# Kernel tuning notes

Measured on AMD Instinct MI355X. Metric: run time of the kernel, lower is better.

## Reference

```python
import jax, jax.numpy as jnp
import numpy as np

B, S, D, H = 2, 2048, 768, 12
DK = D // H
NEG = -10000.0


def setup_inputs() -> dict:
    key = jax.random.key(0)
    ks = jax.random.split(key, 12)
    def lin(k):
        kw, kb = jax.random.split(k)
        return (jax.random.normal(kw, (D, D), jnp.float32) * 0.02,
                jax.random.normal(kb, (D,), jnp.float32) * 0.02)
    Wq, bq = lin(ks[0]); Wk, bk = lin(ks[1]); Wv, bv = lin(ks[2]); Wo, bo = lin(ks[3])
    query = jax.random.normal(ks[4], (B, S, D), jnp.float32)
    key_t = jax.random.normal(ks[5], (B, S, D), jnp.float32)
    value = jax.random.normal(ks[6], (B, S, D), jnp.float32)
    # causal mask, broadcastable to [B,H,S,S]; positions with 0 are masked
    mask = jnp.tril(jnp.ones((S, S), jnp.int32))[None, None, :, :]
    return {"query": query, "key": key_t, "value": value, "mask": mask,
            "Wq": Wq, "bq": bq, "Wk": Wk, "bk": bk, "Wv": Wv, "bv": bv,
            "Wo": Wo, "bo": bo}


def reference(query, key, value, mask, Wq, bq, Wk, bk, Wv, bv, Wo, bo):
    # torch.nn.Linear: y = x @ W^T + b
    def split_heads(x):  # [B,S,D] -> [B,H,S,DK]
        return x.reshape(B, S, H, DK).transpose(0, 2, 1, 3)
    q = split_heads(query @ Wq.T + bq)
    k = split_heads(key @ Wk.T + bk)
    v = split_heads(value @ Wv.T + bv)
    scores = jnp.einsum('bhqd,bhkd->bhqk', q, k) / jnp.sqrt(jnp.float32(DK))
    scores = jnp.where(mask == 0, NEG, scores)  # masked_fill(mask==0, -1e4)
    attn = jax.nn.softmax(scores, axis=-1)      # dropout p=0.0 -> identity
    x = jnp.einsum('bhqk,bhkd->bhqd', attn, v)  # [B,H,S,DK]
    x = x.transpose(0, 2, 1, 3).reshape(B, S, D)
    return x @ Wo.T + bo
```

## Files before the change

kernel.cpp:

```cpp
#include <hip/hip_runtime.h>
#include <cstdint>


#define B_ 2
#define S_ 2048
#define D_ 768
#define H_ 12
#define DK_ 64

typedef __bf16 bf16;
typedef __bf16 bf16x8 __attribute__((ext_vector_type(8)));
typedef float f32x4 __attribute__((ext_vector_type(4)));
typedef uint32_t u32x4 __attribute__((ext_vector_type(4)));
typedef uint16_t u16x4 __attribute__((ext_vector_type(4)));

__device__ __forceinline__ f32x4 mfma16(bf16x8 a, bf16x8 b, f32x4 c) {
  return __builtin_amdgcn_mfma_f32_16x16x32_bf16(a, b, c, 0, 0, 0);
}

__device__ __forceinline__ void gl2lds16(const bf16* g, bf16* l) {
  __builtin_amdgcn_global_load_lds(
      (const __attribute__((address_space(1))) uint32_t*)g,
      (__attribute__((address_space(3))) uint32_t*)l, 16, 0, 0);
}

struct raw8 { u32x4 a, b; };

__device__ __forceinline__ raw8 fetch8(const void* base, size_t off, int isbf) {
  raw8 r;
  if (isbf) {
    r.a = *(const u32x4*)((const bf16*)base + off);
  } else {
    const float* f = (const float*)base + off;
    r.a = *(const u32x4*)f;
    r.b = *(const u32x4*)(f + 4);
  }
  return r;
}

__device__ __forceinline__ bf16x8 cvt8(raw8 r, int isbf) {
  if (isbf) return __builtin_bit_cast(bf16x8, r.a);
  const float4 x = __builtin_bit_cast(float4, r.a);
  const float4 y = __builtin_bit_cast(float4, r.b);
  bf16x8 o;
  o[0]=(bf16)x.x; o[1]=(bf16)x.y; o[2]=(bf16)x.z; o[3]=(bf16)x.w;
  o[4]=(bf16)y.x; o[5]=(bf16)y.y; o[6]=(bf16)y.z; o[7]=(bf16)y.w;
  return o;
}

__device__ __forceinline__ float load_scalar(const void* base, int idx, int isbf) {
  return isbf ? (float)((const bf16*)base)[idx] : ((const float*)base)[idx];
}

__device__ __forceinline__ uint32_t pack2bf(float lo, float hi) {
  const uint16_t l = __builtin_bit_cast(uint16_t, (bf16)lo);
  const uint16_t h = __builtin_bit_cast(uint16_t, (bf16)hi);
  return (uint32_t)l | ((uint32_t)h << 16);
}

#define NE_ 3145728
#define NW_ 589824
#define NE8_ 393216
#define NW8_ 73728
__global__ __launch_bounds__(256) void cvt_kernel(
    const void* __restrict__ q, const void* __restrict__ k,
    const void* __restrict__ v,
    const void* __restrict__ Wq, const void* __restrict__ Wk,
    const void* __restrict__ Wv, const void* __restrict__ Wo,
    bf16* __restrict__ dst, int* __restrict__ flag)
{
  __shared__ int cnt;
  if (threadIdx.x == 0) cnt = 0;
  __syncthreads();
  {
    int local = 0;
    const uint32_t* qw = (const uint32_t*)q;
    for (int i = (int)threadIdx.x; i < 1024; i += 256) {
      const uint32_t e = (qw[i] >> 7) & 0xff;
      if (e >= 96 && e <= 140) local++;
    }
    atomicAdd(&cnt, local);
  }
  __syncthreads();
  const int isbf = (cnt >= 600) ? 1 : 0;
  if (blockIdx.x == 0 && threadIdx.x == 0) *flag = isbf;

  const int u = (int)(blockIdx.x * 256 + threadIdx.x);
  if (u >= 3 * NE8_ + 4 * NW8_) return;
  const void* src;
  size_t off8;
  bf16* d;
  if (u < 3 * NE8_) {
    const int wq = u / NE8_;
    off8 = (size_t)(u - wq * NE8_);
    src = (wq == 0) ? q : (wq == 1) ? k : v;
    d = dst + (size_t)wq * NE_;
  } else {
    const int u2 = u - 3 * NE8_;
    const int wq = u2 / NW8_;
    off8 = (size_t)(u2 - wq * NW8_);
    src = (wq == 0) ? Wq : (wq == 1) ? Wk : (wq == 2) ? Wv : Wo;
    d = dst + (size_t)3 * NE_ + (size_t)wq * NW_;
  }
  raw8 rr = fetch8(src, off8 * 8, isbf);
  *(bf16x8*)&d[off8 * 8] = cvt8(rr, isbf);
}

#define GEMM_BODY(Xg, Wg, m0, n0)                                            \
  __shared__ __align__(16) bf16 As[2][128][32];                              \
  __shared__ __align__(16) bf16 Bs[2][128][32];                              \
  const int t = (int)threadIdx.x;                                            \
  const int lane = t & 63, w = t >> 6, c = lane & 15, quad = lane >> 4;      \
  const int wm = w & 1, wn = w >> 1;                                         \
  const int rsub = lane >> 2, csub = (lane & 3) * 8;                         \
  f32x4 acc[4][4];                                                           \
  _Pragma("unroll") for (int i = 0; i < 4; ++i)                              \
      _Pragma("unroll") for (int j = 0; j < 4; ++j)                          \
          _Pragma("unroll") for (int e = 0; e < 4; ++e) acc[i][j][e] = 0.0f; \
  auto issue = [&](int p, int k0) {                                          \
    _Pragma("unroll") for (int i = 0; i < 2; ++i) {                          \
      const int rr = (w * 2 + i) * 16;                                       \
      gl2lds16(Xg + (size_t)(m0 + rr + rsub) * D_ + k0 + csub,               \
               &As[p][rr][0]);                                               \
      gl2lds16(Wg + (size_t)(n0 + rr + rsub) * D_ + k0 + csub,               \
               &Bs[p][rr][0]);                                               \
    }                                                                        \
  };                                                                         \
  issue(0, 0);                                                               \
  int p = 0;                                                                 \
  for (int kt = 0; kt < D_ / 32; ++kt) {                                     \
    __syncthreads();                                                         \
    if (kt + 1 < D_ / 32) issue(p ^ 1, (kt + 1) * 32);                       \
    bf16x8 af[4], bfr[4];                                                    \
    _Pragma("unroll") for (int i = 0; i < 4; ++i) {                          \
      af[i] = *(const bf16x8*)&As[p][wm * 64 + i * 16 + c][quad * 8];        \
      bfr[i] = *(const bf16x8*)&Bs[p][wn * 64 + i * 16 + c][quad * 8];       \
    }                                                                        \
    _Pragma("unroll") for (int i = 0; i < 4; ++i)                            \
        _Pragma("unroll") for (int j = 0; j < 4; ++j)                        \
            acc[i][j] = mfma16(af[i], bfr[j], acc[i][j]);                    \
    p ^= 1;                                                                  \
  }

__global__ __launch_bounds__(256) void qkv_kernel(
    const bf16* __restrict__ qc, const bf16* __restrict__ kc,
    const bf16* __restrict__ vc,
    const bf16* __restrict__ Wqc, const bf16* __restrict__ Wkc,
    const bf16* __restrict__ Wvc,
    const void* __restrict__ bq, const void* __restrict__ bk,
    const void* __restrict__ bv,
    bf16* __restrict__ qh, bf16* __restrict__ kh, bf16* __restrict__ vt,
    const int* __restrict__ flag)
{
  const int isbf = *flag;
  const int z = (int)blockIdx.y / 6;
  const int n0 = ((int)blockIdx.y % 6) * 128;
  const int m0 = (int)blockIdx.x * 128;
  const bf16* Xg = (z == 0) ? qc : (z == 1) ? kc : vc;
  const bf16* Wg = (z == 0) ? Wqc : (z == 1) ? Wkc : Wvc;
  const void* bias = (z == 0) ? bq : (z == 1) ? bk : bv;
  bf16* out = (z == 0) ? qh : (z == 1) ? kh : vt;

  GEMM_BODY(Xg, Wg, m0, n0)

#pragma unroll
  for (int j = 0; j < 4; ++j) {
    const int n = n0 + wn * 64 + j * 16 + c;
    const int h = n >> 6, dk = n & 63;
    const float bv_ = load_scalar(bias, n, isbf);
#pragma unroll
    for (int i = 0; i < 4; ++i)
#pragma unroll
      for (int r = 0; r < 4; ++r) {
        const int m = m0 + wm * 64 + i * 16 + quad * 4 + r;
        const int bi = m >> 11, s = m & (S_ - 1);
        const float val = acc[i][j][r] + bv_;
        if (z != 2)
          out[(((size_t)bi * H_ + h) * S_ + s) * DK_ + dk] = (bf16)val;
        else
          out[(((size_t)bi * H_ + h) * DK_ + dk) * S_ + s] = (bf16)val;
      }
  }
}

__global__ __launch_bounds__(256) void oproj_kernel(
    const bf16* __restrict__ xh, const bf16* __restrict__ Woc,
    const void* __restrict__ bias, void* __restrict__ out,
    const int* __restrict__ flag)
{
  const int isbf = *flag;
  const int m0 = (int)blockIdx.x * 128;
  const int n0 = (int)blockIdx.y * 128;

  GEMM_BODY(xh, Woc, m0, n0)

#pragma unroll
  for (int j = 0; j < 4; ++j) {
    const int n = n0 + wn * 64 + j * 16 + c;
    const float bv_ = load_scalar(bias, n, isbf);
#pragma unroll
    for (int i = 0; i < 4; ++i)
#pragma unroll
      for (int r = 0; r < 4; ++r) {
        const int m = m0 + wm * 64 + i * 16 + quad * 4 + r;
        const float v = acc[i][j][r] + bv_;
        if (isbf) ((bf16*)out)[(size_t)m * D_ + n] = (bf16)v;
        else      ((float*)out)[(size_t)m * D_ + n] = v;
      }
  }
}

__global__ __launch_bounds__(256) void attn_kernel(
    const bf16* __restrict__ qh, const bf16* __restrict__ kh,
    const bf16* __restrict__ vt, bf16* __restrict__ xh)
{
  __shared__ __align__(16) bf16 Ks[2][64][72];
  __shared__ __align__(16) bf16 Vts[2][64][72];

  const int g = (int)blockIdx.y >> 3;
  const int x = (int)blockIdx.x;
  const int jt = (g == 0) ? x : (g == 1) ? (31 - x) : (x ^ 16);
  const int qb = jt * 64;

  const int bh = (int)blockIdx.y;
  const int bi = bh / H_, h = bh % H_;
  const bf16* qp = qh + (size_t)bh * S_ * DK_;
  const bf16* kp = kh + (size_t)bh * S_ * DK_;
  const bf16* vp = vt + (size_t)bh * DK_ * S_;

  const int t = (int)threadIdx.x;
  const int lane = t & 63, w = t >> 6, c = lane & 15, quad = lane >> 4;
  const int r8 = t >> 3, sg = t & 7;

  const float SCL = 0.125f * 1.44269504088896f;
  bf16x8 qB0 = *(const bf16x8*)(qp + (size_t)(qb + w * 16 + c) * DK_ + quad * 8);
  bf16x8 qB1 = *(const bf16x8*)(qp + (size_t)(qb + w * 16 + c) * DK_ + 32 + quad * 8);
#pragma unroll
  for (int i = 0; i < 8; ++i) {
    qB0[i] = (bf16)((float)qB0[i] * SCL);
    qB1[i] = (bf16)((float)qB1[i] * SCL);
  }

  f32x4 accT[4];
#pragma unroll
  for (int nb = 0; nb < 4; ++nb)
#pragma unroll
    for (int i = 0; i < 4; ++i) accT[nb][i] = 0.0f;
  float lp = 0.0f;

  bf16x8 kr0, kr1, vr0, vr1;
  auto loadKV = [&](int kb) {
    kr0 = *(const bf16x8*)(kp + (size_t)(kb + r8) * DK_ + sg * 8);
    kr1 = *(const bf16x8*)(kp + (size_t)(kb + 32 + r8) * DK_ + sg * 8);
    vr0 = *(const bf16x8*)(vp + (size_t)r8 * S_ + kb + sg * 8);
    vr1 = *(const bf16x8*)(vp + (size_t)(r8 + 32) * S_ + kb + sg * 8);
  };

  const int nkt = jt + 1;
  loadKV(0);
  int p = 0;

  for (int kt = 0; kt < nkt; ++kt) {
    *(bf16x8*)&Ks[p][r8][sg * 8]       = kr0;
    *(bf16x8*)&Ks[p][32 + r8][sg * 8]  = kr1;
    *(bf16x8*)&Vts[p][r8][sg * 8]      = vr0;
    *(bf16x8*)&Vts[p][32 + r8][sg * 8] = vr1;
    __syncthreads();
    if (kt + 1 < nkt) loadKV((kt + 1) * 64);
    const bool diag = (kt == nkt - 1);

#pragma unroll
    for (int gq = 0; gq < 2; ++gq) {
      float sv[2][4];
#pragma unroll
      for (int tt = 0; tt < 2; ++tt) {
        const int kl = gq * 32 + tt * 16;
        f32x4 st;
#pragma unroll
        for (int i = 0; i < 4; ++i) st[i] = 0.0f;
        const bf16x8 ka0 = *(const bf16x8*)&Ks[p][kl + c][quad * 8];
        const bf16x8 ka1 = *(const bf16x8*)&Ks[p][kl + c][32 + quad * 8];
        st = mfma16(ka0, qB0, st);
        st = mfma16(ka1, qB1, st);
        if (diag) {
#pragma unroll
          for (int r = 0; r < 4; ++r)
            if (kl + quad * 4 + r > w * 16 + c) st[r] = -__builtin_inff();
        }
#pragma unroll
        for (int r = 0; r < 4; ++r) sv[tt][r] = exp2f(st[r]);
        lp += (sv[tt][0] + sv[tt][1]) + (sv[tt][2] + sv[tt][3]);
      }
      const uint32_t p00 = pack2bf(sv[0][0], sv[0][1]);
      const uint32_t p01 = pack2bf(sv[0][2], sv[0][3]);
      const uint32_t p10 = pack2bf(sv[1][0], sv[1][1]);
      const uint32_t p11 = pack2bf(sv[1][2], sv[1][3]);
      const int aLo = (32 * (quad & 1) + c) * 4;
      const int aHi = aLo + 64;
      const bool tt0 = (quad < 2);
      u32x4 bu;
      {
        const uint32_t t0 = (uint32_t)__builtin_amdgcn_ds_bpermute(aLo, (int)p00);
        const uint32_t t1 = (uint32_t)__builtin_amdgcn_ds_bpermute(aLo, (int)p10);
        bu[0] = tt0 ? t0 : t1;
        const uint32_t t2 = (uint32_t)__builtin_amdgcn_ds_bpermute(aLo, (int)p01);
        const uint32_t t3 = (uint32_t)__builtin_amdgcn_ds_bpermute(aLo, (int)p11);
        bu[1] = tt0 ? t2 : t3;
        const uint32_t t4 = (uint32_t)__builtin_amdgcn_ds_bpermute(aHi, (int)p00);
        const uint32_t t5 = (uint32_t)__builtin_amdgcn_ds_bpermute(aHi, (int)p10);
        bu[2] = tt0 ? t4 : t5;
        const uint32_t t6 = (uint32_t)__builtin_amdgcn_ds_bpermute(aHi, (int)p01);
        const uint32_t t7 = (uint32_t)__builtin_amdgcn_ds_bpermute(aHi, (int)p11);
        bu[3] = tt0 ? t6 : t7;
      }
      const bf16x8 pfrag = __builtin_bit_cast(bf16x8, bu);
#pragma unroll
      for (int nb = 0; nb < 4; ++nb) {
        const bf16x8 vf = *(const bf16x8*)&Vts[p][nb * 16 + c][gq * 32 + quad * 8];
        accT[nb] = mfma16(vf, pfrag, accT[nb]);
      }
    }
    p ^= 1;
  }

  float l = lp;
  l += __shfl_xor(l, 16);
  l += __shfl_xor(l, 32);
  const float inv = 1.0f / l;
  const int s = qb + w * 16 + c;
  bf16* xr = xh + ((size_t)bi * S_ + s) * D_ + h * DK_;
#pragma unroll
  for (int nb = 0; nb < 4; ++nb) {
    u16x4 pk;
#pragma unroll
    for (int r = 0; r < 4; ++r)
      pk[r] = __builtin_bit_cast(uint16_t, (bf16)(accT[nb][r] * inv));
    *(u16x4*)&xr[nb * 16 + quad * 4] = pk;
  }
}

extern "C" void kernel_launch(void* const* d_in, const int* in_sizes, int n_in,
                              void* d_out, int out_size, void* d_ws, size_t ws_size,
                              hipStream_t stream) {
  const void* query = d_in[0];
  const void* key_  = d_in[1];
  const void* value = d_in[2];
  const void* Wq = d_in[4];
  const void* bq = d_in[5];
  const void* Wk = d_in[6];
  const void* bk = d_in[7];
  const void* Wv = d_in[8];
  const void* bv = d_in[9];
  const void* Wo = d_in[10];
  const void* bo = d_in[11];

  bf16* qc  = (bf16*)d_ws;
  bf16* kc  = qc + NE_;
  bf16* vc  = kc + NE_;
  bf16* Wqc = vc + NE_;
  bf16* Wkc = Wqc + NW_;
  bf16* Wvc = Wkc + NW_;
  bf16* Woc = Wvc + NW_;
  bf16* qh  = Woc + NW_;
  bf16* kh  = qh + NE_;
  bf16* vt  = kh + NE_;
  bf16* xh  = qc;
  int* flag = (int*)(vt + NE_);

  dim3 blk(256);
  cvt_kernel<<<(3 * NE8_ + 4 * NW8_ + 255) / 256, blk, 0, stream>>>(
      query, key_, value, Wq, Wk, Wv, Wo, qc, flag);
  qkv_kernel<<<dim3(32, 18), blk, 0, stream>>>(
      qc, kc, vc, Wqc, Wkc, Wvc, bq, bk, bv, qh, kh, vt, flag);
  attn_kernel<<<dim3(32, 24), blk, 0, stream>>>(qh, kh, vt, xh);
  oproj_kernel<<<dim3(32, 6), blk, 0, stream>>>(xh, Woc, bo, d_out, flag);
}
```

Measured before the change: 229.7 us.

## Fuse input conversion into GEMMs and add persistent work-stealing attention scheduler

Removes the separate fp32-to-bf16 conversion kernel. The QKV and output-projection GEMMs now load raw inputs through registers, convert them, and store to padded LDS, replacing the direct global-to-LDS loads. The attention kernel becomes a persistent kernel that pulls items from an atomic counter, largest causal tiles first, to balance load. The V transpose store is vectorised. Risks: the register-staged loads lose the async LDS path, and the atomic scheduler relies on the counter being reset by the prior kernel.

New measurement: 250.9 us. +9.2%, slower.

```diff
diff --git a/kernel.cpp b/kernel.cpp
--- a/kernel.cpp
+++ b/kernel.cpp
@@ -7,6 +7,7 @@
 #define D_ 768
 #define H_ 12
 #define DK_ 64
+#define NITEMS 768
 
 typedef __bf16 bf16;
 typedef __bf16 bf16x8 __attribute__((ext_vector_type(8)));
@@ -16,12 +17,6 @@
 
 __device__ __forceinline__ f32x4 mfma16(bf16x8 a, bf16x8 b, f32x4 c) {
   return __builtin_amdgcn_mfma_f32_16x16x32_bf16(a, b, c, 0, 0, 0);
-}
-
-__device__ __forceinline__ void gl2lds16(const bf16* g, bf16* l) {
-  __builtin_amdgcn_global_load_lds(
-      (const __attribute__((address_space(1))) uint32_t*)g,
-      (__attribute__((address_space(3))) uint32_t*)l, 16, 0, 0);
 }
 
 struct raw8 { u32x4 a, b; };
@@ -58,79 +53,48 @@
   return (uint32_t)l | ((uint32_t)h << 16);
 }
 
-#define NE_ 3145728
-#define NW_ 589824
-#define NE8_ 393216
-#define NW8_ 73728
-__global__ __launch_bounds__(256) void cvt_kernel(
-    const void* __restrict__ q, const void* __restrict__ k,
-    const void* __restrict__ v,
-    const void* __restrict__ Wq, const void* __restrict__ Wk,
-    const void* __restrict__ Wv, const void* __restrict__ Wo,
-    bf16* __restrict__ dst, int* __restrict__ flag)
-{
+__device__ __forceinline__ int sniff(const void* q) {
   __shared__ int cnt;
   if (threadIdx.x == 0) cnt = 0;
   __syncthreads();
-  {
-    int local = 0;
-    const uint32_t* qw = (const uint32_t*)q;
-    for (int i = (int)threadIdx.x; i < 1024; i += 256) {
-      const uint32_t e = (qw[i] >> 7) & 0xff;
-      if (e >= 96 && e <= 140) local++;
-    }
-    atomicAdd(&cnt, local);
-  }
+  int local = 0;
+  const uint32_t* qw = (const uint32_t*)q;
+  for (int i = (int)threadIdx.x; i < 1024; i += 256) {
+    const uint32_t e = (qw[i] >> 7) & 0xff;
+    if (e >= 96 && e <= 140) local++;
+  }
+  atomicAdd(&cnt, local);
   __syncthreads();
-  const int isbf = (cnt >= 600) ? 1 : 0;
-  if (blockIdx.x == 0 && threadIdx.x == 0) *flag = isbf;
-
-  const int u = (int)(blockIdx.x * 256 + threadIdx.x);
-  if (u >= 3 * NE8_ + 4 * NW8_) return;
-  const void* src;
-  size_t off8;
-  bf16* d;
-  if (u < 3 * NE8_) {
-    const int wq = u / NE8_;
-    off8 = (size_t)(u - wq * NE8_);
-    src = (wq == 0) ? q : (wq == 1) ? k : v;
-    d = dst + (size_t)wq * NE_;
-  } else {
-    const int u2 = u - 3 * NE8_;
-    const int wq = u2 / NW8_;
-    off8 = (size_t)(u2 - wq * NW8_);
-    src = (wq == 0) ? Wq : (wq == 1) ? Wk : (wq == 2) ? Wv : Wo;
-    d = dst + (size_t)3 * NE_ + (size_t)wq * NW_;
-  }
-  raw8 rr = fetch8(src, off8 * 8, isbf);
-  *(bf16x8*)&d[off8 * 8] = cvt8(rr, isbf);
-}
-
-#define GEMM_BODY(Xg, Wg, m0, n0)                                            \
-  __shared__ __align__(16) bf16 As[2][128][32];                              \
-  __shared__ __align__(16) bf16 Bs[2][128][32];                              \
+  return (cnt >= 600) ? 1 : 0;
+}
+
+#define GEMM_CVT(Xg, xbf, Wg, wbf, m0, n0)                                   \
+  __shared__ __align__(16) bf16 As[2][128][40];                              \
+  __shared__ __align__(16) bf16 Bs[2][128][40];                              \
   const int t = (int)threadIdx.x;                                            \
   const int lane = t & 63, w = t >> 6, c = lane & 15, quad = lane >> 4;      \
   const int wm = w & 1, wn = w >> 1;                                         \
-  const int rsub = lane >> 2, csub = (lane & 3) * 8;                         \
+  const int srow = t >> 1, scol = (t & 1) * 16;                              \
   f32x4 acc[4][4];                                                           \
   _Pragma("unroll") for (int i = 0; i < 4; ++i)                              \
       _Pragma("unroll") for (int j = 0; j < 4; ++j)                          \
           _Pragma("unroll") for (int e = 0; e < 4; ++e) acc[i][j][e] = 0.0f; \
-  auto issue = [&](int p, int k0) {                                          \
-    _Pragma("unroll") for (int i = 0; i < 2; ++i) {                          \
-      const int rr = (w * 2 + i) * 16;                                       \
-      gl2lds16(Xg + (size_t)(m0 + rr + rsub) * D_ + k0 + csub,               \
-               &As[p][rr][0]);                                               \
-      gl2lds16(Wg + (size_t)(n0 + rr + rsub) * D_ + k0 + csub,               \
-               &Bs[p][rr][0]);                                               \
+  raw8 pa[2], pb[2];                                                         \
+  auto fetchAB = [&](int k0) {                                               \
+    _Pragma("unroll") for (int u = 0; u < 2; ++u) {                          \
+      pa[u] = fetch8(Xg, (size_t)(m0 + srow) * D_ + k0 + scol + u * 8, xbf); \
+      pb[u] = fetch8(Wg, (size_t)(n0 + srow) * D_ + k0 + scol + u * 8, wbf); \
     }                                                                        \
   };                                                                         \
-  issue(0, 0);                                                               \
+  fetchAB(0);                                                                \
   int p = 0;                                                                 \
   for (int kt = 0; kt < D_ / 32; ++kt) {                                     \
+    _Pragma("unroll") for (int u = 0; u < 2; ++u) {                          \
+      *(bf16x8*)&As[p][srow][scol + u * 8] = cvt8(pa[u], xbf);               \
+      *(bf16x8*)&Bs[p][srow][scol + u * 8] = cvt8(pb[u], wbf);               \
+    }                                                                        \
     __syncthreads();                                                         \
-    if (kt + 1 < D_ / 32) issue(p ^ 1, (kt + 1) * 32);                       \
+    if (kt + 1 < D_ / 32) fetchAB((kt + 1) * 32);                            \
     bf16x8 af[4], bfr[4];                                                    \
     _Pragma("unroll") for (int i = 0; i < 4; ++i) {                          \
       af[i] = *(const bf16x8*)&As[p][wm * 64 + i * 16 + c][quad * 8];        \
@@ -143,48 +107,62 @@
   }
 
 __global__ __launch_bounds__(256) void qkv_kernel(
-    const bf16* __restrict__ qc, const bf16* __restrict__ kc,
-    const bf16* __restrict__ vc,
-    const bf16* __restrict__ Wqc, const bf16* __restrict__ Wkc,
-    const bf16* __restrict__ Wvc,
+    const void* __restrict__ q, const void* __restrict__ k,
+    const void* __restrict__ v,
+    const void* __restrict__ Wq, const void* __restrict__ Wk,
+    const void* __restrict__ Wv,
     const void* __restrict__ bq, const void* __restrict__ bk,
     const void* __restrict__ bv,
     bf16* __restrict__ qh, bf16* __restrict__ kh, bf16* __restrict__ vt,
-    const int* __restrict__ flag)
+    int* __restrict__ flag, int* __restrict__ ctr)
 {
-  const int isbf = *flag;
+  const int isbf = sniff(q);
+  if (blockIdx.x == 0 && blockIdx.y == 0 && threadIdx.x == 0) {
+    *flag = isbf;
+    *ctr = 0;
+  }
   const int z = (int)blockIdx.y / 6;
   const int n0 = ((int)blockIdx.y % 6) * 128;
   const int m0 = (int)blockIdx.x * 128;
-  const bf16* Xg = (z == 0) ? qc : (z == 1) ? kc : vc;
-  const bf16* Wg = (z == 0) ? Wqc : (z == 1) ? Wkc : Wvc;
+  const void* Xg = (z == 0) ? q : (z == 1) ? k : v;
+  const void* Wg = (z == 0) ? Wq : (z == 1) ? Wk : Wv;
   const void* bias = (z == 0) ? bq : (z == 1) ? bk : bv;
   bf16* out = (z == 0) ? qh : (z == 1) ? kh : vt;
 
-  GEMM_BODY(Xg, Wg, m0, n0)
+  GEMM_CVT(Xg, isbf, Wg, isbf, m0, n0)
 
 #pragma unroll
   for (int j = 0; j < 4; ++j) {
     const int n = n0 + wn * 64 + j * 16 + c;
     const int h = n >> 6, dk = n & 63;
     const float bv_ = load_scalar(bias, n, isbf);
-#pragma unroll
-    for (int i = 0; i < 4; ++i)
-#pragma unroll
-      for (int r = 0; r < 4; ++r) {
-        const int m = m0 + wm * 64 + i * 16 + quad * 4 + r;
-        const int bi = m >> 11, s = m & (S_ - 1);
-        const float val = acc[i][j][r] + bv_;
-        if (z != 2)
-          out[(((size_t)bi * H_ + h) * S_ + s) * DK_ + dk] = (bf16)val;
-        else
-          out[(((size_t)bi * H_ + h) * DK_ + dk) * S_ + s] = (bf16)val;
+    if (z != 2) {
+#pragma unroll
+      for (int i = 0; i < 4; ++i)
+#pragma unroll
+        for (int r = 0; r < 4; ++r) {
+          const int m = m0 + wm * 64 + i * 16 + quad * 4 + r;
+          const int bi = m >> 11, s = m & (S_ - 1);
+          out[(((size_t)bi * H_ + h) * S_ + s) * DK_ + dk] =
+              (bf16)(acc[i][j][r] + bv_);
+        }
+    } else {
+#pragma unroll
+      for (int i = 0; i < 4; ++i) {
+        const int m = m0 + wm * 64 + i * 16 + quad * 4;
+        const int bi = m >> 11, s0 = m & (S_ - 1);
+        u16x4 pk;
+#pragma unroll
+        for (int r = 0; r < 4; ++r)
+          pk[r] = __builtin_bit_cast(uint16_t, (bf16)(acc[i][j][r] + bv_));
+        *(u16x4*)&out[(((size_t)bi * H_ + h) * DK_ + dk) * S_ + s0] = pk;
       }
+    }
   }
 }
 
 __global__ __launch_bounds__(256) void oproj_kernel(
-    const bf16* __restrict__ xh, const bf16* __restrict__ Woc,
+    const bf16* __restrict__ xh, const void* __restrict__ Wo,
     const void* __restrict__ bias, void* __restrict__ out,
     const int* __restrict__ flag)
 {
@@ -192,7 +170,7 @@
   const int m0 = (int)blockIdx.x * 128;
   const int n0 = (int)blockIdx.y * 128;
 
-  GEMM_BODY(xh, Woc, m0, n0)
+  GEMM_CVT(xh, 1, Wo, isbf, m0, n0)
 
 #pragma unroll
   for (int j = 0; j < 4; ++j) {
@@ -212,130 +190,135 @@
 
 __global__ __launch_bounds__(256) void attn_kernel(
     const bf16* __restrict__ qh, const bf16* __restrict__ kh,
-    const bf16* __restrict__ vt, bf16* __restrict__ xh)
+    const bf16* __restrict__ vt, bf16* __restrict__ xh,
+    int* __restrict__ ctr)
 {
   __shared__ __align__(16) bf16 Ks[2][64][72];
   __shared__ __align__(16) bf16 Vts[2][64][72];
-
-  const int g = (int)blockIdx.y >> 3;
-  const int x = (int)blockIdx.x;
-  const int jt = (g == 0) ? x : (g == 1) ? (31 - x) : (x ^ 16);
-  const int qb = jt * 64;
-
-  const int bh = (int)blockIdx.y;
-  const int bi = bh / H_, h = bh % H_;
-  const bf16* qp = qh + (size_t)bh * S_ * DK_;
-  const bf16* kp = kh + (size_t)bh * S_ * DK_;
-  const bf16* vp = vt + (size_t)bh * DK_ * S_;
+  __shared__ int s_item;
 
   const int t = (int)threadIdx.x;
   const int lane = t & 63, w = t >> 6, c = lane & 15, quad = lane >> 4;
   const int r8 = t >> 3, sg = t & 7;
-
   const float SCL = 0.125f * 1.44269504088896f;
-  bf16x8 qB0 = *(const bf16x8*)(qp + (size_t)(qb + w * 16 + c) * DK_ + quad * 8);
-  bf16x8 qB1 = *(const bf16x8*)(qp + (size_t)(qb + w * 16 + c) * DK_ + 32 + quad * 8);
-#pragma unroll
-  for (int i = 0; i < 8; ++i) {
-    qB0[i] = (bf16)((float)qB0[i] * SCL);
-    qB1[i] = (bf16)((float)qB1[i] * SCL);
-  }
-
-  f32x4 accT[4];
-#pragma unroll
-  for (int nb = 0; nb < 4; ++nb)
-#pragma unroll
-    for (int i = 0; i < 4; ++i) accT[nb][i] = 0.0f;
-  float lp = 0.0f;
-
-  bf16x8 kr0, kr1, vr0, vr1;
-  auto loadKV = [&](int kb) {
-    kr0 = *(const bf16x8*)(kp + (size_t)(kb + r8) * DK_ + sg * 8);
-    kr1 = *(const bf16x8*)(kp + (size_t)(kb + 32 + r8) * DK_ + sg * 8);
-    vr0 = *(const bf16x8*)(vp + (size_t)r8 * S_ + kb + sg * 8);
-    vr1 = *(const bf16x8*)(vp + (size_t)(r8 + 32) * S_ + kb + sg * 8);
-  };
-
-  const int nkt = jt + 1;
-  loadKV(0);
-  int p = 0;
-
-  for (int kt = 0; kt < nkt; ++kt) {
-    *(bf16x8*)&Ks[p][r8][sg * 8]       = kr0;
-    *(bf16x8*)&Ks[p][32 + r8][sg * 8]  = kr1;
-    *(bf16x8*)&Vts[p][r8][sg * 8]      = vr0;
-    *(bf16x8*)&Vts[p][32 + r8][sg * 8] = vr1;
+
+  for (;;) {
+    if (t == 0) s_item = atomicAdd(ctr, 1);
     __syncthreads();
-    if (kt + 1 < nkt) loadKV((kt + 1) * 64);
-    const bool diag = (kt == nkt - 1);
-
-#pragma unroll
-    for (int gq = 0; gq < 2; ++gq) {
-      float sv[2][4];
-#pragma unroll
-      for (int tt = 0; tt < 2; ++tt) {
-        const int kl = gq * 32 + tt * 16;
-        f32x4 st;
-#pragma unroll
-        for (int i = 0; i < 4; ++i) st[i] = 0.0f;
-        const bf16x8 ka0 = *(const bf16x8*)&Ks[p][kl + c][quad * 8];
-        const bf16x8 ka1 = *(const bf16x8*)&Ks[p][kl + c][32 + quad * 8];
-        st = mfma16(ka0, qB0, st);
-        st = mfma16(ka1, qB1, st);
-        if (diag) {
-#pragma unroll
-          for (int r = 0; r < 4; ++r)
-            if (kl + quad * 4 + r > w * 16 + c) st[r] = -__builtin_inff();
+    const int item = s_item;
+    if (item >= NITEMS) break;
+    const int jt = 31 - item / 24;
+    const int bh = item % 24;
+    const int qb = jt * 64;
+    const int bi = bh / H_, h = bh % H_;
+    const bf16* qp = qh + (size_t)bh * S_ * DK_;
+    const bf16* kp = kh + (size_t)bh * S_ * DK_;
+    const bf16* vp = vt + (size_t)bh * DK_ * S_;
+
+    bf16x8 qB0 = *(const bf16x8*)(qp + (size_t)(qb + w * 16 + c) * DK_ + quad * 8);
+    bf16x8 qB1 = *(const bf16x8*)(qp + (size_t)(qb + w * 16 + c) * DK_ + 32 + quad * 8);
+#pragma unroll
+    for (int i = 0; i < 8; ++i) {
+      qB0[i] = (bf16)((float)qB0[i] * SCL);
+      qB1[i] = (bf16)((float)qB1[i] * SCL);
+    }
+
+    f32x4 accT[4];
+#pragma unroll
+    for (int nb = 0; nb < 4; ++nb)
+#pragma unroll
+      for (int i = 0; i < 4; ++i) accT[nb][i] = 0.0f;
+    float lp = 0.0f;
+
+    bf16x8 kr0, kr1, vr0, vr1;
+    auto loadKV = [&](int kb) {
+      kr0 = *(const bf16x8*)(kp + (size_t)(kb + r8) * DK_ + sg * 8);
+      kr1 = *(const bf16x8*)(kp + (size_t)(kb + 32 + r8) * DK_ + sg * 8);
+      vr0 = *(const bf16x8*)(vp + (size_t)r8 * S_ + kb + sg * 8);
+      vr1 = *(const bf16x8*)(vp + (size_t)(r8 + 32) * S_ + kb + sg * 8);
+    };
+
+    const int nkt = jt + 1;
+    loadKV(0);
+    int p = 0;
+
+    for (int kt = 0; kt < nkt; ++kt) {
+      *(bf16x8*)&Ks[p][r8][sg * 8]       = kr0;
+      *(bf16x8*)&Ks[p][32 + r8][sg * 8]  = kr1;
+      *(bf16x8*)&Vts[p][r8][sg * 8]      = vr0;
+      *(bf16x8*)&Vts[p][32 + r8][sg * 8] = vr1;
+      __syncthreads();
+      if (kt + 1 < nkt) loadKV((kt + 1) * 64);
+      const bool diag = (kt == nkt - 1);
+
+#pragma unroll
+      for (int gq = 0; gq < 2; ++gq) {
+        float sv[2][4];
+#pragma unroll
+        for (int tt = 0; tt < 2; ++tt) {
+          const int kl = gq * 32 + tt * 16;
+          f32x4 st;
+#pragma unroll
+          for (int i = 0; i < 4; ++i) st[i] = 0.0f;
+          const bf16x8 ka0 = *(const bf16x8*)&Ks[p][kl + c][quad * 8];
+          const bf16x8 ka1 = *(const bf16x8*)&Ks[p][kl + c][32 + quad * 8];
+          st = mfma16(ka0, qB0, st);
+          st = mfma16(ka1, qB1, st);
+          if (diag) {
+#pragma unroll
+            for (int r = 0; r < 4; ++r)
+              if (kl + quad * 4 + r > w * 16 + c) st[r] = -__builtin_inff();
+          }
+#pragma unroll
+          for (int r = 0; r < 4; ++r) sv[tt][r] = exp2f(st[r]);
+          lp += (sv[tt][0] + sv[tt][1]) + (sv[tt][2] + sv[tt][3]);
         }
-#pragma unroll
-        for (int r = 0; r < 4; ++r) sv[tt][r] = exp2f(st[r]);
-        lp += (sv[tt][0] + sv[tt][1]) + (sv[tt][2] + sv[tt][3]);
+        const uint32_t p00 = pack2bf(sv[0][0], sv[0][1]);
+        const uint32_t p01 = pack2bf(sv[0][2], sv[0][3]);
+        const uint32_t p10 = pack2bf(sv[1][0], sv[1][1]);
+        const uint32_t p11 = pack2bf(sv[1][2], sv[1][3]);
+        const int aLo = (32 * (quad & 1) + c) * 4;
+        const int aHi = aLo + 64;
+        const bool tt0 = (quad < 2);
+        u32x4 bu;
+        {
+          const uint32_t t0 = (uint32_t)__builtin_amdgcn_ds_bpermute(aLo, (int)p00);
+          const uint32_t t1 = (uint32_t)__builtin_amdgcn_ds_bpermute(aLo, (int)p10);
+          bu[0] = tt0 ? t0 : t1;
+          const uint32_t t2 = (uint32_t)__builtin_amdgcn_ds_bpermute(aLo, (int)p01);
+          const uint32_t t3 = (uint32_t)__builtin_amdgcn_ds_bpermute(aLo, (int)p11);
+          bu[1] = tt0 ? t2 : t3;
+          const uint32_t t4 = (uint32_t)__builtin_amdgcn_ds_bpermute(aHi, (int)p00);
+          const uint32_t t5 = (uint32_t)__builtin_amdgcn_ds_bpermute(aHi, (int)p10);
+          bu[2] = tt0 ? t4 : t5;
+          const uint32_t t6 = (uint32_t)__builtin_amdgcn_ds_bpermute(aHi, (int)p01);
+          const uint32_t t7 = (uint32_t)__builtin_amdgcn_ds_bpermute(aHi, (int)p11);
+          bu[3] = tt0 ? t6 : t7;
+        }
+        const bf16x8 pfrag = __builtin_bit_cast(bf16x8, bu);
+#pragma unroll
+        for (int nb = 0; nb < 4; ++nb) {
+          const bf16x8 vf = *(const bf16x8*)&Vts[p][nb * 16 + c][gq * 32 + quad * 8];
+          accT[nb] = mfma16(vf, pfrag, accT[nb]);
+        }
       }
-      const uint32_t p00 = pack2bf(sv[0][0], sv[0][1]);
-      const uint32_t p01 = pack2bf(sv[0][2], sv[0][3]);
-      const uint32_t p10 = pack2bf(sv[1][0], sv[1][1]);
-      const uint32_t p11 = pack2bf(sv[1][2], sv[1][3]);
-      const int aLo = (32 * (quad & 1) + c) * 4;
-      const int aHi = aLo + 64;
-      const bool tt0 = (quad < 2);
-      u32x4 bu;
-      {
-        const uint32_t t0 = (uint32_t)__builtin_amdgcn_ds_bpermute(aLo, (int)p00);
-        const uint32_t t1 = (uint32_t)__builtin_amdgcn_ds_bpermute(aLo, (int)p10);
-        bu[0] = tt0 ? t0 : t1;
-        const uint32_t t2 = (uint32_t)__builtin_amdgcn_ds_bpermute(aLo, (int)p01);
-        const uint32_t t3 = (uint32_t)__builtin_amdgcn_ds_bpermute(aLo, (int)p11);
-        bu[1] = tt0 ? t2 : t3;
-        const uint32_t t4 = (uint32_t)__builtin_amdgcn_ds_bpermute(aHi, (int)p00);
-        const uint32_t t5 = (uint32_t)__builtin_amdgcn_ds_bpermute(aHi, (int)p10);
-        bu[2] = tt0 ? t4 : t5;
-        const uint32_t t6 = (uint32_t)__builtin_amdgcn_ds_bpermute(aHi, (int)p01);
-        const uint32_t t7 = (uint32_t)__builtin_amdgcn_ds_bpermute(aHi, (int)p11);
-        bu[3] = tt0 ? t6 : t7;
-      }
-      const bf16x8 pfrag = __builtin_bit_cast(bf16x8, bu);
-#pragma unroll
-      for (int nb = 0; nb < 4; ++nb) {
-        const bf16x8 vf = *(const bf16x8*)&Vts[p][nb * 16 + c][gq * 32 + quad * 8];
-        accT[nb] = mfma16(vf, pfrag, accT[nb]);
-      }
+      p ^= 1;
     }
-    p ^= 1;
-  }
-
-  float l = lp;
-  l += __shfl_xor(l, 16);
-  l += __shfl_xor(l, 32);
-  const float inv = 1.0f / l;
-  const int s = qb + w * 16 + c;
-  bf16* xr = xh + ((size_t)bi * S_ + s) * D_ + h * DK_;
-#pragma unroll
-  for (int nb = 0; nb < 4; ++nb) {
-    u16x4 pk;
-#pragma unroll
-    for (int r = 0; r < 4; ++r)
-      pk[r] = __builtin_bit_cast(uint16_t, (bf16)(accT[nb][r] * inv));
-    *(u16x4*)&xr[nb * 16 + quad * 4] = pk;
+
+    float l = lp;
+    l += __shfl_xor(l, 16);
+    l += __shfl_xor(l, 32);
+    const float inv = 1.0f / l;
+    const int s = qb + w * 16 + c;
+    bf16* xr = xh + ((size_t)bi * S_ + s) * D_ + h * DK_;
+#pragma unroll
+    for (int nb = 0; nb < 4; ++nb) {
+      u16x4 pk;
+#pragma unroll
+      for (int r = 0; r < 4; ++r)
+        pk[r] = __builtin_bit_cast(uint16_t, (bf16)(accT[nb][r] * inv));
+      *(u16x4*)&xr[nb * 16 + quad * 4] = pk;
+    }
   }
 }
 
@@ -354,24 +337,17 @@
   const void* Wo = d_in[10];
   const void* bo = d_in[11];
 
-  bf16* qc  = (bf16*)d_ws;
-  bf16* kc  = qc + NE_;
-  bf16* vc  = kc + NE_;
-  bf16* Wqc = vc + NE_;
-  bf16* Wkc = Wqc + NW_;
-  bf16* Wvc = Wkc + NW_;
-  bf16* Woc = Wvc + NW_;
-  bf16* qh  = Woc + NW_;
-  bf16* kh  = qh + NE_;
-  bf16* vt  = kh + NE_;
-  bf16* xh  = qc;
-  int* flag = (int*)(vt + NE_);
+  const size_t NE = (size_t)B_ * H_ * S_ * DK_;
+  bf16* qh  = (bf16*)d_ws;
+  bf16* kh  = qh + NE;
+  bf16* vt  = kh + NE;
+  bf16* xh  = vt + NE;
+  int* flag = (int*)(xh + NE);
+  int* ctr  = flag + 1;
 
   dim3 blk(256);
-  cvt_kernel<<<(3 * NE8_ + 4 * NW8_ + 255) / 256, blk, 0, stream>>>(
-      query, key_, value, Wq, Wk, Wv, Wo, qc, flag);
   qkv_kernel<<<dim3(32, 18), blk, 0, stream>>>(
-      qc, kc, vc, Wqc, Wkc, Wvc, bq, bk, bv, qh, kh, vt, flag);
-  attn_kernel<<<dim3(32, 24), blk, 0, stream>>>(qh, kh, vt, xh);
-  oproj_kernel<<<dim3(32, 6), blk, 0, stream>>>(xh, Woc, bo, d_out, flag);
-}
+      query, key_, value, Wq, Wk, Wv, bq, bk, bv, qh, kh, vt, flag, ctr);
+  attn_kernel<<<dim3(1024), blk, 0, stream>>>(qh, kh, vt, xh, ctr);
+  oproj_kernel<<<dim3(32, 6), blk, 0, stream>>>(xh, Wo, bo, d_out, flag);
+}
```
